# Performance work log

Hardware: AMD Instinct MI355X
Metric: run time of the kernel (lower is better)

The kernel has to match this reference:

```python
import jax, jax.numpy as jnp
import numpy as np
from jax import lax

EPS = 1e-5
TEM = 10.0  # self.tem at init; tem_proportion buffer is 0 so it stays 10.0


def _conv1d(x, w, padding, dilation=1, groups=1):
    # x: [B, C, S], w: [O, I//groups, K]
    return lax.conv_general_dilated(
        x, w, window_strides=(1,), padding=[(padding, padding)],
        rhs_dilation=(dilation,), dimension_numbers=('NCH', 'OIH', 'NCH'),
        feature_group_count=groups)


def _bn(y, gamma, beta):
    # training-mode BatchNorm1d: stats over (batch, length) per channel
    m = y.mean(axis=(0, 2), keepdims=True)
    v = y.var(axis=(0, 2), keepdims=True)
    return (y - m) * lax.rsqrt(v + EPS) * gamma[None, :, None] + beta[None, :, None]


def _nor_conv(x, w, g, b, k):
    return _bn(_conv1d(jax.nn.relu(x), w, padding=k // 2), g, b)


def _dil_conv(x, wd, wp, g, b, k):
    C = x.shape[1]
    y = _conv1d(jax.nn.relu(x), wd, padding=k - 1, dilation=2, groups=C)
    y = _conv1d(y, wp, padding=0)
    return _bn(y, g, b)


def _avg_pool3(x):
    s = lax.reduce_window(x, 0.0, lax.add, (1, 1, 3), (1, 1, 1),
                          [(0, 0), (0, 0), (1, 1)])
    return s / 3.0  # count_include_pad=True


def _max_pool3(x):
    return lax.reduce_window(x, -jnp.inf, lax.max, (1, 1, 3), (1, 1, 1),
                             [(0, 0), (0, 0), (1, 1)])


def _forward(x, u, arch_parameters,
             w_nor3, g_nor3, b_nor3, w_nor5, g_nor5, b_nor5,
             w_nor7, g_nor7, b_nor7,
             wd_dil3, wp_dil3, g_dil3, b_dil3,
             wd_dil5, wp_dil5, g_dil5, b_dil5,
             wd_dil7, wp_dil7, g_dil7, b_dil7):
    # ---- Gumbel straight-through gate (get_gumbel_prob) ----
    uc = jnp.clip(u, 1e-9, 1.0 - 1e-9)
    gumbels = -jnp.log(-jnp.log(uc))  # -log(Exp(1) sample)
    logits = (jax.nn.log_softmax(arch_parameters, axis=1) + gumbels) / TEM
    probs = jax.nn.softmax(logits, axis=1)          # [1, 10]
    index = jnp.argmax(probs, axis=-1)              # [1]
    one_h = jax.nn.one_hot(index, probs.shape[-1], dtype=probs.dtype)
    hardwts = one_h - lax.stop_gradient(probs) + probs  # straight-through

    # ---- forward_gdas: single edge (max_nodes=2) ----
    xc = jnp.transpose(x, (0, 2, 1))  # [B, H, S]: hidden=channels, seq=length
    branches = [
        lambda t: jnp.zeros_like(t),                         # none
        _avg_pool3,                                          # avg_pool_3
        _max_pool3,                                          # max_pool_3
        lambda t: _nor_conv(t, w_nor3, g_nor3, b_nor3, 3),   # nor_conv_3
        lambda t: _nor_conv(t, w_nor5, g_nor5, b_nor5, 5),   # nor_conv_5
        lambda t: _nor_conv(t, w_nor7, g_nor7, b_nor7, 7),   # nor_conv_7
        lambda t: _dil_conv(t, wd_dil3, wp_dil3, g_dil3, b_dil3, 3),
        lambda t: _dil_conv(t, wd_dil5, wp_dil5, g_dil5, b_dil5, 5),
        lambda t: _dil_conv(t, wd_dil7, wp_dil7, g_dil7, b_dil7, 7),
        lambda t: t,                                         # skip_connect
    ]
    idx = index[0]
    w = hardwts[0]                                  # [10]
    sel = lax.switch(idx, branches, xc)             # only argmax op is run
    w_sel = jnp.take(w, idx)
    # GDAS: w[argmax]*op(x) + sum of remaining scalar weights (broadcast add)
    out = w_sel * sel + (jnp.sum(w) - w_sel)
    out = jnp.transpose(out, (0, 2, 1))             # back to [B, S, H]
    return out + x                                  # residual


def setup_inputs() -> dict:
    key = jax.random.key(0)
    ks = jax.random.split(key, 16)
    B, S, H = 8, 512, 768
    d = {
        'x': jax.random.normal(ks[0], (B, S, H), jnp.float32),
        'u': jax.random.uniform(ks[1], (1, 10), jnp.float32),
        'arch_parameters': 0.001 * jax.random.normal(ks[2], (1, 10), jnp.float32),
    }
    i = 3
    for k in (3, 5, 7):
        d[f'w_nor{k}'] = 0.02 * jax.random.normal(ks[i], (H, H, k), jnp.float32); i += 1
        d[f'g_nor{k}'] = jnp.ones((H,), jnp.float32)
        d[f'b_nor{k}'] = jnp.zeros((H,), jnp.float32)
    for k in (3, 5, 7):
        d[f'wd_dil{k}'] = 0.1 * jax.random.normal(ks[i], (H, 1, k), jnp.float32); i += 1
        d[f'wp_dil{k}'] = 0.02 * jax.random.normal(ks[i], (H, H, 1), jnp.float32); i += 1
        d[f'g_dil{k}'] = jnp.ones((H,), jnp.float32)
        d[f'b_dil{k}'] = jnp.zeros((H,), jnp.float32)
    return d


def reference(x, u, arch_parameters,
              w_nor3, g_nor3, b_nor3, w_nor5, g_nor5, b_nor5,
              w_nor7, g_nor7, b_nor7,
              wd_dil3, wp_dil3, g_dil3, b_dil3,
              wd_dil5, wp_dil5, g_dil5, b_dil5,
              wd_dil7, wp_dil7, g_dil7, b_dil7):
    return _forward(x, u, arch_parameters,
                    w_nor3, g_nor3, b_nor3, w_nor5, g_nor5, b_nor5,
                    w_nor7, g_nor7, b_nor7,
                    wd_dil3, wp_dil3, g_dil3, b_dil3,
                    wd_dil5, wp_dil5, g_dil5, b_dil5,
                    wd_dil7, wp_dil7, g_dil7, b_dil7)
```

## Files before the change

### kernel.cpp

```cpp
#include <hip/hip_runtime.h>
#include <math.h>

#define BB 8
#define SS 512
#define HH 768
#define NTOT (BB*SS*HH)
#define EPSBN 1e-5f

typedef __attribute__((ext_vector_type(8))) short short8v;
typedef __attribute__((ext_vector_type(4))) float float4v;

struct Params {
  const float *x, *u, *ap;
  const float *w_nor3, *g_nor3, *b_nor3;
  const float *w_nor5, *g_nor5, *b_nor5;
  const float *w_nor7, *g_nor7, *b_nor7;
  const float *wd3, *wp3, *gd3, *bd3;
  const float *wd5, *wp5, *gd5, *bd5;
  const float *wd7, *wp7, *gd7, *bd7;
  float *out;
  float *hdr;
  float *y;
  float *z;
  float *psum;
  float *psq;
  float *mbuf;
  float *ibuf;
};

__device__ __forceinline__ short f2bf(float f) {
  union { float f; unsigned u; } v; v.f = f;
  unsigned r = v.u + 0x7FFF + ((v.u >> 16) & 1);
  return (short)(r >> 16);
}

__global__ void gate_kernel(Params p) {
  if (threadIdx.x != 0 || blockIdx.x != 0) return;
  float ap[10], lg[10], pr[10];
  float mx = -INFINITY;
  for (int i = 0; i < 10; i++) { ap[i] = p.ap[i]; mx = fmaxf(mx, ap[i]); }
  float se = 0.f;
  for (int i = 0; i < 10; i++) se += expf(ap[i] - mx);
  float lse = mx + logf(se);
  float lmax = -INFINITY;
  for (int i = 0; i < 10; i++) {
    float uc = fminf(fmaxf(p.u[i], 1e-9f), 1.f - 1e-9f);
    float gb = -logf(-logf(uc));
    lg[i] = ((ap[i] - lse) + gb) * 0.1f;
    lmax = fmaxf(lmax, lg[i]);
  }
  float ps = 0.f;
  for (int i = 0; i < 10; i++) { pr[i] = expf(lg[i] - lmax); ps += pr[i]; }
  int idx = 0; float best = -INFINITY;
  for (int i = 0; i < 10; i++) {
    pr[i] /= ps;
    if (pr[i] > best) { best = pr[i]; idx = i; }
  }
  float w_sel = (1.0f - pr[idx]) + pr[idx];
  p.hdr[0] = w_sel;
  p.hdr[1] = 0.0f;
  ((int*)p.hdr)[2] = idx;
}

__global__ __launch_bounds__(256) void dw_kernel(Params p) {
  int idx = ((const int*)p.hdr)[2];
  if (idx < 6 || idx > 8) return;
  int k = 3 + 2 * (idx - 6);
  const float* wd = (idx == 6) ? p.wd3 : (idx == 7) ? p.wd5 : p.wd7;
  int tid = blockIdx.x * 256 + threadIdx.x;
  if (tid >= NTOT) return;
  int c = tid % HH;
  int bs = tid / HH;
  int s = bs % SS;
  int b = bs / SS;
  float acc = 0.f;
  for (int dk = 0; dk < k; dk++) {
    int ss = s + 2 * dk - (k - 1);
    if (ss >= 0 && ss < SS) {
      float v = p.x[((size_t)(b * SS + ss)) * HH + c];
      acc += fmaxf(v, 0.f) * wd[c * k + dk];
    }
  }
  p.z[tid] = acc;
}

#define BM 128
#define BN 64
#define BK 32
#define LROW 40
__global__ __launch_bounds__(256) void conv_gemm_kernel(Params p) {
  int idx = ((const int*)p.hdr)[2];
  if (idx < 3 || idx > 8) return;
  bool nor = (idx <= 5);
  int k = nor ? (3 + 2 * (idx - 3)) : (3 + 2 * (idx - 6));
  const float* W = nor ? ((idx == 3) ? p.w_nor3 : (idx == 4) ? p.w_nor5 : p.w_nor7)
                       : ((idx == 6) ? p.wp3 : (idx == 7) ? p.wp5 : p.wp7);
  const float* A = nor ? p.x : p.z;
  int taps = nor ? k : 1;
  int halo = nor ? (k >> 1) : 0;

  __shared__ __attribute__((aligned(16))) short As[BM * LROW];
  __shared__ __attribute__((aligned(16))) short Bs[BN * LROW];

  int mt = blockIdx.x;
  int b = mt >> 2;
  int s0 = (mt & 3) * BM;
  int o0 = blockIdx.y * BN;

  int t = threadIdx.x;
  int lane = t & 63;
  int wid = t >> 6;
  int wm0 = (wid >> 1) * 64;
  int wn0 = (wid & 1) * 32;
  int l16 = lane & 15;
  int quad = lane >> 4;

  int sa_m = t >> 1;
  int sa_h = t & 1;
  int sb_n = t >> 2;
  int sb_seg = t & 3;

  float4v acc[4][2];
#pragma unroll
  for (int mi = 0; mi < 4; mi++)
#pragma unroll
    for (int ni = 0; ni < 2; ni++) acc[mi][ni] = (float4v){0.f, 0.f, 0.f, 0.f};

  for (int dk = 0; dk < taps; dk++) {
    int shift = dk - halo;
    for (int k0 = 0; k0 < HH; k0 += BK) {
      {
        int srow = s0 + sa_m + shift;
        float4 f[4];
        if (srow >= 0 && srow < SS) {
          const float* ap = A + ((size_t)(b * SS + srow)) * HH + k0 + sa_h * 16;
#pragma unroll
          for (int j = 0; j < 4; j++) f[j] = ((const float4*)ap)[j];
        } else {
#pragma unroll
          for (int j = 0; j < 4; j++) f[j] = (float4){0.f, 0.f, 0.f, 0.f};
        }
        short h16[16];
#pragma unroll
        for (int j = 0; j < 4; j++) {
          float vx = f[j].x, vy = f[j].y, vz = f[j].z, vw = f[j].w;
          if (nor) { vx = fmaxf(vx, 0.f); vy = fmaxf(vy, 0.f); vz = fmaxf(vz, 0.f); vw = fmaxf(vw, 0.f); }
          h16[4 * j + 0] = f2bf(vx); h16[4 * j + 1] = f2bf(vy);
          h16[4 * j + 2] = f2bf(vz); h16[4 * j + 3] = f2bf(vw);
        }
        short* dst = &As[sa_m * LROW + sa_h * 16];
        *(short8v*)dst = *(short8v*)&h16[0];
        *(short8v*)(dst + 8) = *(short8v*)&h16[8];
      }
      {
        short h8[8];
        int o = o0 + sb_n;
        if (!nor) {
          const float* bp = W + (size_t)o * HH + k0 + sb_seg * 8;
          float4 f0 = ((const float4*)bp)[0];
          float4 f1 = ((const float4*)bp)[1];
          h8[0] = f2bf(f0.x); h8[1] = f2bf(f0.y); h8[2] = f2bf(f0.z); h8[3] = f2bf(f0.w);
          h8[4] = f2bf(f1.x); h8[5] = f2bf(f1.y); h8[6] = f2bf(f1.z); h8[7] = f2bf(f1.w);
        } else {
#pragma unroll
          for (int j = 0; j < 8; j++) {
            int i = k0 + sb_seg * 8 + j;
            h8[j] = f2bf(W[((size_t)o * HH + i) * k + dk]);
          }
        }
        *(short8v*)&Bs[sb_n * LROW + sb_seg * 8] = *(short8v*)&h8[0];
      }
      __syncthreads();

      short8v af[4], bf[2];
#pragma unroll
      for (int mi = 0; mi < 4; mi++)
        af[mi] = *(const short8v*)&As[(wm0 + mi * 16 + l16) * LROW + quad * 8];
#pragma unroll
      for (int ni = 0; ni < 2; ni++)
        bf[ni] = *(const short8v*)&Bs[(wn0 + ni * 16 + l16) * LROW + quad * 8];
#pragma unroll
      for (int mi = 0; mi < 4; mi++)
#pragma unroll
        for (int ni = 0; ni < 2; ni++)
          acc[mi][ni] = __builtin_amdgcn_mfma_f32_16x16x32_bf16(af[mi], bf[ni], acc[mi][ni], 0, 0, 0);
      __syncthreads();
    }
  }

#pragma unroll
  for (int mi = 0; mi < 4; mi++) {
#pragma unroll
    for (int ni = 0; ni < 2; ni++) {
      int col = o0 + wn0 + ni * 16 + l16;
#pragma unroll
      for (int r = 0; r < 4; r++) {
        int row = s0 + wm0 + mi * 16 + quad * 4 + r;
        p.y[((size_t)(b * SS + row)) * HH + col] = acc[mi][ni][r];
      }
    }
  }
}

__global__ __launch_bounds__(256) void bn_stats1(Params p) {
  int idx = ((const int*)p.hdr)[2];
  if (idx < 3 || idx > 8) return;
  int t = threadIdx.x;
  int c = blockIdx.y * 64 + (t & 63);
  int rsub = t >> 6;
  float s = 0.f, q = 0.f;
  int rbase = blockIdx.x * 256 + rsub;
  for (int j = 0; j < 64; j++) {
    float v = p.y[(size_t)(rbase + 4 * j) * HH + c];
    s += v; q += v * v;
  }
  __shared__ float red[2][4][64];
  red[0][rsub][t & 63] = s;
  red[1][rsub][t & 63] = q;
  __syncthreads();
  if (t < 64) {
    float ts = red[0][0][t] + red[0][1][t] + red[0][2][t] + red[0][3][t];
    float tq = red[1][0][t] + red[1][1][t] + red[1][2][t] + red[1][3][t];
    p.psum[blockIdx.x * HH + blockIdx.y * 64 + t] = ts;
    p.psq[blockIdx.x * HH + blockIdx.y * 64 + t] = tq;
  }
}

__global__ __launch_bounds__(256) void bn_stats2(Params p) {
  int idx = ((const int*)p.hdr)[2];
  if (idx < 3 || idx > 8) return;
  int c = blockIdx.x * 256 + threadIdx.x;
  if (c >= HH) return;
  float s = 0.f, q = 0.f;
  for (int j = 0; j < 16; j++) { s += p.psum[j * HH + c]; q += p.psq[j * HH + c]; }
  float mean = s * (1.f / 4096.f);
  float var = q * (1.f / 4096.f) - mean * mean;
  p.mbuf[c] = mean;
  p.ibuf[c] = rsqrtf(var + EPSBN);
}

__global__ __launch_bounds__(256) void epilogue_kernel(Params p) {
  int idx = ((const int*)p.hdr)[2];
  float w_sel = p.hdr[0], w_rest = p.hdr[1];
  int tid = blockIdx.x * 256 + threadIdx.x;
  if (tid >= NTOT) return;
  float xv = p.x[tid];
  float sel;
  if (idx >= 3 && idx <= 8) {
    const float* g = (idx == 3) ? p.g_nor3 : (idx == 4) ? p.g_nor5 : (idx == 5) ? p.g_nor7
                   : (idx == 6) ? p.gd3 : (idx == 7) ? p.gd5 : p.gd7;
    const float* be = (idx == 3) ? p.b_nor3 : (idx == 4) ? p.b_nor5 : (idx == 5) ? p.b_nor7
                    : (idx == 6) ? p.bd3 : (idx == 7) ? p.bd5 : p.bd7;
    int h = tid % HH;
    float yv = p.y[tid];
    sel = (yv - p.mbuf[h]) * p.ibuf[h] * g[h] + be[h];
  } else if (idx == 0) {
    sel = 0.f;
  } else if (idx == 9) {
    sel = xv;
  } else {
    int bs = tid / HH;
    int s = bs % SS;
    if (idx == 1) {
      float xm = (s > 0) ? p.x[tid - HH] : 0.f;
      float xp = (s < SS - 1) ? p.x[tid + HH] : 0.f;
      sel = (xm + xv + xp) * (1.f / 3.f);
    } else {
      float xm = (s > 0) ? p.x[tid - HH] : -INFINITY;
      float xp = (s < SS - 1) ? p.x[tid + HH] : -INFINITY;
      sel = fmaxf(fmaxf(xm, xv), xp);
    }
  }
  p.out[tid] = w_sel * sel + w_rest + xv;
}

extern "C" void kernel_launch(void* const* d_in, const int* in_sizes, int n_in,
                              void* d_out, int out_size, void* d_ws, size_t ws_size,
                              hipStream_t stream) {
  Params p;
  p.x = (const float*)d_in[0];
  p.u = (const float*)d_in[1];
  p.ap = (const float*)d_in[2];
  p.w_nor3 = (const float*)d_in[3];  p.g_nor3 = (const float*)d_in[4];  p.b_nor3 = (const float*)d_in[5];
  p.w_nor5 = (const float*)d_in[6];  p.g_nor5 = (const float*)d_in[7];  p.b_nor5 = (const float*)d_in[8];
  p.w_nor7 = (const float*)d_in[9];  p.g_nor7 = (const float*)d_in[10]; p.b_nor7 = (const float*)d_in[11];
  p.wd3 = (const float*)d_in[12]; p.wp3 = (const float*)d_in[13]; p.gd3 = (const float*)d_in[14]; p.bd3 = (const float*)d_in[15];
  p.wd5 = (const float*)d_in[16]; p.wp5 = (const float*)d_in[17]; p.gd5 = (const float*)d_in[18]; p.bd5 = (const float*)d_in[19];
  p.wd7 = (const float*)d_in[20]; p.wp7 = (const float*)d_in[21]; p.gd7 = (const float*)d_in[22]; p.bd7 = (const float*)d_in[23];
  p.out = (float*)d_out;

  char* ws = (char*)d_ws;
  size_t off = 0;
  p.hdr = (float*)(ws + off); off += 256;
  p.y   = (float*)(ws + off); off += (size_t)NTOT * 4;
  p.z   = (float*)(ws + off); off += (size_t)NTOT * 4;
  p.psum = (float*)(ws + off); off += 16 * HH * 4;
  p.psq  = (float*)(ws + off); off += 16 * HH * 4;
  p.mbuf = (float*)(ws + off); off += HH * 4;
  p.ibuf = (float*)(ws + off); off += HH * 4;

  int nblk = (NTOT + 255) / 256;

  hipLaunchKernelGGL(gate_kernel, dim3(1), dim3(64), 0, stream, p);
  hipLaunchKernelGGL(dw_kernel, dim3(nblk), dim3(256), 0, stream, p);
  hipLaunchKernelGGL(conv_gemm_kernel, dim3(32, HH / BN), dim3(256), 0, stream, p);
  hipLaunchKernelGGL(bn_stats1, dim3(16, HH / 64), dim3(256), 0, stream, p);
  hipLaunchKernelGGL(bn_stats2, dim3((HH + 255) / 256), dim3(256), 0, stream, p);
  hipLaunchKernelGGL(epilogue_kernel, dim3(nblk), dim3(256), 0, stream, p);
}
```

Baseline: 144.7 us.

## Merge all stages into one cooperative persistent kernel with grid syncs

Replaces the six separate launches (gate, depthwise, GEMM, two BN-stat passes, epilogue) with a single cooperative kernel of 512 blocks that recomputes the Gumbel gate in every block and separates phases with grid-wide syncs. For the parameter-free branches it skips the GEMM and BN work entirely and writes output in one vectorized pass. The GEMM tile shrinks from 128x64 to 64x64 and is scheduled persistently over 768 tiles, and the elementwise passes use float4. Grid syncs and the smaller tiles with less reuse could offset the savings from fewer launches.

New measurement: 176.1 us. +21.7%, slower.

```diff
diff --git a/kernel.cpp b/kernel.cpp
--- a/kernel.cpp
+++ b/kernel.cpp
@@ -1,11 +1,18 @@
 #include <hip/hip_runtime.h>
+#include <hip/hip_cooperative_groups.h>
 #include <math.h>
+
+namespace cg = cooperative_groups;
 
 #define BB 8
 #define SS 512
 #define HH 768
+#define H4 (HH/4)
 #define NTOT (BB*SS*HH)
+#define N4 (NTOT/4)
 #define EPSBN 1e-5f
+#define GRID 512
+#define TPB 256
 
 typedef __attribute__((ext_vector_type(8))) short short8v;
 typedef __attribute__((ext_vector_type(4))) float float4v;
@@ -19,7 +26,6 @@
   const float *wd5, *wp5, *gd5, *bd5;
   const float *wd7, *wp7, *gd7, *bd7;
   float *out;
-  float *hdr;
   float *y;
   float *z;
   float *psum;
@@ -34,244 +40,253 @@
   return (short)(r >> 16);
 }
 
-__global__ void gate_kernel(Params p) {
-  if (threadIdx.x != 0 || blockIdx.x != 0) return;
-  float ap[10], lg[10], pr[10];
+__global__ __launch_bounds__(TPB, 2) void nas_coop(Params p) {
+  cg::grid_group gg = cg::this_grid();
+  int t = threadIdx.x;
+  int bid = blockIdx.x;
+
+  float apv[10], lg[10], pr[10];
   float mx = -INFINITY;
-  for (int i = 0; i < 10; i++) { ap[i] = p.ap[i]; mx = fmaxf(mx, ap[i]); }
+#pragma unroll
+  for (int i = 0; i < 10; i++) { apv[i] = p.ap[i]; mx = fmaxf(mx, apv[i]); }
   float se = 0.f;
-  for (int i = 0; i < 10; i++) se += expf(ap[i] - mx);
+#pragma unroll
+  for (int i = 0; i < 10; i++) se += expf(apv[i] - mx);
   float lse = mx + logf(se);
   float lmax = -INFINITY;
+#pragma unroll
   for (int i = 0; i < 10; i++) {
     float uc = fminf(fmaxf(p.u[i], 1e-9f), 1.f - 1e-9f);
     float gb = -logf(-logf(uc));
-    lg[i] = ((ap[i] - lse) + gb) * 0.1f;
+    lg[i] = ((apv[i] - lse) + gb) * 0.1f;
     lmax = fmaxf(lmax, lg[i]);
   }
   float ps = 0.f;
+#pragma unroll
   for (int i = 0; i < 10; i++) { pr[i] = expf(lg[i] - lmax); ps += pr[i]; }
   int idx = 0; float best = -INFINITY;
+#pragma unroll
   for (int i = 0; i < 10; i++) {
     pr[i] /= ps;
     if (pr[i] > best) { best = pr[i]; idx = i; }
   }
   float w_sel = (1.0f - pr[idx]) + pr[idx];
-  p.hdr[0] = w_sel;
-  p.hdr[1] = 0.0f;
-  ((int*)p.hdr)[2] = idx;
-}
-
-__global__ __launch_bounds__(256) void dw_kernel(Params p) {
-  int idx = ((const int*)p.hdr)[2];
-  if (idx < 6 || idx > 8) return;
-  int k = 3 + 2 * (idx - 6);
-  const float* wd = (idx == 6) ? p.wd3 : (idx == 7) ? p.wd5 : p.wd7;
-  int tid = blockIdx.x * 256 + threadIdx.x;
-  if (tid >= NTOT) return;
-  int c = tid % HH;
-  int bs = tid / HH;
-  int s = bs % SS;
-  int b = bs / SS;
-  float acc = 0.f;
-  for (int dk = 0; dk < k; dk++) {
-    int ss = s + 2 * dk - (k - 1);
-    if (ss >= 0 && ss < SS) {
-      float v = p.x[((size_t)(b * SS + ss)) * HH + c];
-      acc += fmaxf(v, 0.f) * wd[c * k + dk];
-    }
-  }
-  p.z[tid] = acc;
-}
-
-#define BM 128
-#define BN 64
-#define BK 32
-#define LROW 40
-__global__ __launch_bounds__(256) void conv_gemm_kernel(Params p) {
-  int idx = ((const int*)p.hdr)[2];
-  if (idx < 3 || idx > 8) return;
+
+  const float4* x4 = (const float4*)p.x;
+  float4* o4 = (float4*)p.out;
+
+  if (idx < 3 || idx > 8) {
+    for (int i = bid * TPB + t; i < N4; i += GRID * TPB) {
+      float4 xv = x4[i];
+      float4 sel;
+      if (idx == 0) {
+        sel = make_float4(0.f, 0.f, 0.f, 0.f);
+      } else if (idx == 9) {
+        sel = xv;
+      } else {
+        int row = i / H4;
+        int s = row % SS;
+        if (idx == 1) {
+          float4 xm = (s > 0) ? x4[i - H4] : make_float4(0.f, 0.f, 0.f, 0.f);
+          float4 xp = (s < SS - 1) ? x4[i + H4] : make_float4(0.f, 0.f, 0.f, 0.f);
+          sel.x = (xm.x + xv.x + xp.x) * (1.f / 3.f);
+          sel.y = (xm.y + xv.y + xp.y) * (1.f / 3.f);
+          sel.z = (xm.z + xv.z + xp.z) * (1.f / 3.f);
+          sel.w = (xm.w + xv.w + xp.w) * (1.f / 3.f);
+        } else {
+          float4 xm = (s > 0) ? x4[i - H4] : make_float4(-INFINITY, -INFINITY, -INFINITY, -INFINITY);
+          float4 xp = (s < SS - 1) ? x4[i + H4] : make_float4(-INFINITY, -INFINITY, -INFINITY, -INFINITY);
+          sel.x = fmaxf(fmaxf(xm.x, xv.x), xp.x);
+          sel.y = fmaxf(fmaxf(xm.y, xv.y), xp.y);
+          sel.z = fmaxf(fmaxf(xm.z, xv.z), xp.z);
+          sel.w = fmaxf(fmaxf(xm.w, xv.w), xp.w);
+        }
+      }
+      float4 ov;
+      ov.x = w_sel * sel.x + xv.x;
+      ov.y = w_sel * sel.y + xv.y;
+      ov.z = w_sel * sel.z + xv.z;
+      ov.w = w_sel * sel.w + xv.w;
+      o4[i] = ov;
+    }
+    return;
+  }
+
   bool nor = (idx <= 5);
   int k = nor ? (3 + 2 * (idx - 3)) : (3 + 2 * (idx - 6));
+
+  __shared__ __attribute__((aligned(16))) short lds[2 * 64 * 40];
+  short* As = lds;
+  short* Bs = lds + 64 * 40;
+
+  if (!nor) {
+    const float* wd = (idx == 6) ? p.wd3 : (idx == 7) ? p.wd5 : p.wd7;
+    float4* z4 = (float4*)p.z;
+    for (int i = bid * TPB + t; i < N4; i += GRID * TPB) {
+      int row = i / H4;
+      int c0 = (i - row * H4) * 4;
+      int s = row % SS;
+      int b = row / SS;
+      float4 acc = make_float4(0.f, 0.f, 0.f, 0.f);
+      for (int dk = 0; dk < k; dk++) {
+        int ss = s + 2 * dk - (k - 1);
+        if (ss >= 0 && ss < SS) {
+          float4 xv = x4[(b * SS + ss) * H4 + (c0 >> 2)];
+          acc.x += fmaxf(xv.x, 0.f) * wd[(c0 + 0) * k + dk];
+          acc.y += fmaxf(xv.y, 0.f) * wd[(c0 + 1) * k + dk];
+          acc.z += fmaxf(xv.z, 0.f) * wd[(c0 + 2) * k + dk];
+          acc.w += fmaxf(xv.w, 0.f) * wd[(c0 + 3) * k + dk];
+        }
+      }
+      z4[i] = acc;
+    }
+    gg.sync();
+  }
+
   const float* W = nor ? ((idx == 3) ? p.w_nor3 : (idx == 4) ? p.w_nor5 : p.w_nor7)
                        : ((idx == 6) ? p.wp3 : (idx == 7) ? p.wp5 : p.wp7);
   const float* A = nor ? p.x : p.z;
   int taps = nor ? k : 1;
   int halo = nor ? (k >> 1) : 0;
 
-  __shared__ __attribute__((aligned(16))) short As[BM * LROW];
-  __shared__ __attribute__((aligned(16))) short Bs[BN * LROW];
-
-  int mt = blockIdx.x;
-  int b = mt >> 2;
-  int s0 = (mt & 3) * BM;
-  int o0 = blockIdx.y * BN;
-
-  int t = threadIdx.x;
-  int lane = t & 63;
-  int wid = t >> 6;
-  int wm0 = (wid >> 1) * 64;
-  int wn0 = (wid & 1) * 32;
-  int l16 = lane & 15;
-  int quad = lane >> 4;
-
-  int sa_m = t >> 1;
-  int sa_h = t & 1;
-  int sb_n = t >> 2;
-  int sb_seg = t & 3;
-
-  float4v acc[4][2];
-#pragma unroll
-  for (int mi = 0; mi < 4; mi++)
-#pragma unroll
-    for (int ni = 0; ni < 2; ni++) acc[mi][ni] = (float4v){0.f, 0.f, 0.f, 0.f};
-
-  for (int dk = 0; dk < taps; dk++) {
-    int shift = dk - halo;
-    for (int k0 = 0; k0 < HH; k0 += BK) {
-      {
-        int srow = s0 + sa_m + shift;
-        float4 f[4];
-        if (srow >= 0 && srow < SS) {
-          const float* ap = A + ((size_t)(b * SS + srow)) * HH + k0 + sa_h * 16;
-#pragma unroll
-          for (int j = 0; j < 4; j++) f[j] = ((const float4*)ap)[j];
-        } else {
-#pragma unroll
-          for (int j = 0; j < 4; j++) f[j] = (float4){0.f, 0.f, 0.f, 0.f};
-        }
-        short h16[16];
-#pragma unroll
-        for (int j = 0; j < 4; j++) {
-          float vx = f[j].x, vy = f[j].y, vz = f[j].z, vw = f[j].w;
-          if (nor) { vx = fmaxf(vx, 0.f); vy = fmaxf(vy, 0.f); vz = fmaxf(vz, 0.f); vw = fmaxf(vw, 0.f); }
-          h16[4 * j + 0] = f2bf(vx); h16[4 * j + 1] = f2bf(vy);
-          h16[4 * j + 2] = f2bf(vz); h16[4 * j + 3] = f2bf(vw);
-        }
-        short* dst = &As[sa_m * LROW + sa_h * 16];
-        *(short8v*)dst = *(short8v*)&h16[0];
-        *(short8v*)(dst + 8) = *(short8v*)&h16[8];
-      }
-      {
-        short h8[8];
-        int o = o0 + sb_n;
-        if (!nor) {
-          const float* bp = W + (size_t)o * HH + k0 + sb_seg * 8;
-          float4 f0 = ((const float4*)bp)[0];
-          float4 f1 = ((const float4*)bp)[1];
+  int lane = t & 63, wid = t >> 6;
+  int wm0 = (wid >> 1) * 32, wn0 = (wid & 1) * 32;
+  int l16 = lane & 15, quad = lane >> 4;
+  int s_row = t >> 2, s_seg = t & 3;
+
+  for (int tile = bid; tile < 64 * 12; tile += GRID) {
+    int mt = tile & 63, nt = tile >> 6;
+    int b = mt >> 3, s0 = (mt & 7) * 64, o0 = nt * 64;
+    float4v acc[2][2];
+#pragma unroll
+    for (int mi = 0; mi < 2; mi++)
+#pragma unroll
+      for (int ni = 0; ni < 2; ni++) acc[mi][ni] = (float4v){0.f, 0.f, 0.f, 0.f};
+
+    for (int dk = 0; dk < taps; dk++) {
+      int shift = dk - halo;
+      for (int k0 = 0; k0 < HH; k0 += 32) {
+        {
+          int srow = s0 + s_row + shift;
+          float4 f0, f1;
+          if (srow >= 0 && srow < SS) {
+            const float* apt = A + ((size_t)(b * SS + srow)) * HH + k0 + s_seg * 8;
+            f0 = ((const float4*)apt)[0];
+            f1 = ((const float4*)apt)[1];
+          } else {
+            f0 = make_float4(0.f, 0.f, 0.f, 0.f);
+            f1 = f0;
+          }
+          if (nor) {
+            f0.x = fmaxf(f0.x, 0.f); f0.y = fmaxf(f0.y, 0.f); f0.z = fmaxf(f0.z, 0.f); f0.w = fmaxf(f0.w, 0.f);
+            f1.x = fmaxf(f1.x, 0.f); f1.y = fmaxf(f1.y, 0.f); f1.z = fmaxf(f1.z, 0.f); f1.w = fmaxf(f1.w, 0.f);
+          }
+          short h8[8];
           h8[0] = f2bf(f0.x); h8[1] = f2bf(f0.y); h8[2] = f2bf(f0.z); h8[3] = f2bf(f0.w);
           h8[4] = f2bf(f1.x); h8[5] = f2bf(f1.y); h8[6] = f2bf(f1.z); h8[7] = f2bf(f1.w);
-        } else {
-#pragma unroll
-          for (int j = 0; j < 8; j++) {
-            int i = k0 + sb_seg * 8 + j;
-            h8[j] = f2bf(W[((size_t)o * HH + i) * k + dk]);
+          *(short8v*)&As[s_row * 40 + s_seg * 8] = *(short8v*)&h8[0];
+        }
+        {
+          int o = o0 + s_row;
+          short hb[8];
+          if (!nor) {
+            const float* bp = W + (size_t)o * HH + k0 + s_seg * 8;
+            float4 g0 = ((const float4*)bp)[0];
+            float4 g1 = ((const float4*)bp)[1];
+            hb[0] = f2bf(g0.x); hb[1] = f2bf(g0.y); hb[2] = f2bf(g0.z); hb[3] = f2bf(g0.w);
+            hb[4] = f2bf(g1.x); hb[5] = f2bf(g1.y); hb[6] = f2bf(g1.z); hb[7] = f2bf(g1.w);
+          } else {
+#pragma unroll
+            for (int j = 0; j < 8; j++)
+              hb[j] = f2bf(W[((size_t)o * HH + k0 + s_seg * 8 + j) * k + dk]);
           }
-        }
-        *(short8v*)&Bs[sb_n * LROW + sb_seg * 8] = *(short8v*)&h8[0];
+          *(short8v*)&Bs[s_row * 40 + s_seg * 8] = *(short8v*)&hb[0];
+        }
+        __syncthreads();
+        short8v af[2], bf[2];
+#pragma unroll
+        for (int mi = 0; mi < 2; mi++)
+          af[mi] = *(const short8v*)&As[(wm0 + mi * 16 + l16) * 40 + quad * 8];
+#pragma unroll
+        for (int ni = 0; ni < 2; ni++)
+          bf[ni] = *(const short8v*)&Bs[(wn0 + ni * 16 + l16) * 40 + quad * 8];
+#pragma unroll
+        for (int mi = 0; mi < 2; mi++)
+#pragma unroll
+          for (int ni = 0; ni < 2; ni++)
+            acc[mi][ni] = __builtin_amdgcn_mfma_f32_16x16x32_bf16(af[mi], bf[ni], acc[mi][ni], 0, 0, 0);
+        __syncthreads();
       }
-      __syncthreads();
-
-      short8v af[4], bf[2];
-#pragma unroll
-      for (int mi = 0; mi < 4; mi++)
-        af[mi] = *(const short8v*)&As[(wm0 + mi * 16 + l16) * LROW + quad * 8];
-#pragma unroll
-      for (int ni = 0; ni < 2; ni++)
-        bf[ni] = *(const short8v*)&Bs[(wn0 + ni * 16 + l16) * LROW + quad * 8];
-#pragma unroll
-      for (int mi = 0; mi < 4; mi++)
-#pragma unroll
-        for (int ni = 0; ni < 2; ni++)
-          acc[mi][ni] = __builtin_amdgcn_mfma_f32_16x16x32_bf16(af[mi], bf[ni], acc[mi][ni], 0, 0, 0);
-      __syncthreads();
-    }
-  }
-
-#pragma unroll
-  for (int mi = 0; mi < 4; mi++) {
-#pragma unroll
-    for (int ni = 0; ni < 2; ni++) {
-      int col = o0 + wn0 + ni * 16 + l16;
-#pragma unroll
-      for (int r = 0; r < 4; r++) {
-        int row = s0 + wm0 + mi * 16 + quad * 4 + r;
-        p.y[((size_t)(b * SS + row)) * HH + col] = acc[mi][ni][r];
+    }
+#pragma unroll
+    for (int mi = 0; mi < 2; mi++)
+#pragma unroll
+      for (int ni = 0; ni < 2; ni++) {
+        int col = o0 + wn0 + ni * 16 + l16;
+#pragma unroll
+        for (int r = 0; r < 4; r++) {
+          int row = s0 + wm0 + mi * 16 + quad * 4 + r;
+          p.y[((size_t)(b * SS + row)) * HH + col] = acc[mi][ni][r];
+        }
       }
-    }
-  }
-}
-
-__global__ __launch_bounds__(256) void bn_stats1(Params p) {
-  int idx = ((const int*)p.hdr)[2];
-  if (idx < 3 || idx > 8) return;
-  int t = threadIdx.x;
-  int c = blockIdx.y * 64 + (t & 63);
-  int rsub = t >> 6;
-  float s = 0.f, q = 0.f;
-  int rbase = blockIdx.x * 256 + rsub;
-  for (int j = 0; j < 64; j++) {
-    float v = p.y[(size_t)(rbase + 4 * j) * HH + c];
-    s += v; q += v * v;
-  }
-  __shared__ float red[2][4][64];
-  red[0][rsub][t & 63] = s;
-  red[1][rsub][t & 63] = q;
-  __syncthreads();
-  if (t < 64) {
-    float ts = red[0][0][t] + red[0][1][t] + red[0][2][t] + red[0][3][t];
-    float tq = red[1][0][t] + red[1][1][t] + red[1][2][t] + red[1][3][t];
-    p.psum[blockIdx.x * HH + blockIdx.y * 64 + t] = ts;
-    p.psq[blockIdx.x * HH + blockIdx.y * 64 + t] = tq;
-  }
-}
-
-__global__ __launch_bounds__(256) void bn_stats2(Params p) {
-  int idx = ((const int*)p.hdr)[2];
-  if (idx < 3 || idx > 8) return;
-  int c = blockIdx.x * 256 + threadIdx.x;
-  if (c >= HH) return;
-  float s = 0.f, q = 0.f;
-  for (int j = 0; j < 16; j++) { s += p.psum[j * HH + c]; q += p.psq[j * HH + c]; }
-  float mean = s * (1.f / 4096.f);
-  float var = q * (1.f / 4096.f) - mean * mean;
-  p.mbuf[c] = mean;
-  p.ibuf[c] = rsqrtf(var + EPSBN);
-}
-
-__global__ __launch_bounds__(256) void epilogue_kernel(Params p) {
-  int idx = ((const int*)p.hdr)[2];
-  float w_sel = p.hdr[0], w_rest = p.hdr[1];
-  int tid = blockIdx.x * 256 + threadIdx.x;
-  if (tid >= NTOT) return;
-  float xv = p.x[tid];
-  float sel;
-  if (idx >= 3 && idx <= 8) {
+  }
+  gg.sync();
+
+  if (bid < 192) {
+    int rchunk = bid & 15, cgp = bid >> 4;
+    int c = cgp * 64 + (t & 63);
+    int rsub = t >> 6;
+    float s_ = 0.f, q = 0.f;
+    int rbase = rchunk * 256 + rsub;
+    for (int j = 0; j < 64; j++) {
+      float v = p.y[(size_t)(rbase + 4 * j) * HH + c];
+      s_ += v; q += v * v;
+    }
+    float* red = (float*)lds;
+    red[(0 * 4 + rsub) * 64 + (t & 63)] = s_;
+    red[(1 * 4 + rsub) * 64 + (t & 63)] = q;
+    __syncthreads();
+    if (t < 64) {
+      float ts = red[t] + red[64 + t] + red[128 + t] + red[192 + t];
+      float tq = red[256 + t] + red[320 + t] + red[384 + t] + red[448 + t];
+      p.psum[rchunk * HH + cgp * 64 + t] = ts;
+      p.psq[rchunk * HH + cgp * 64 + t] = tq;
+    }
+  }
+  gg.sync();
+
+  if (bid < 3) {
+    int c = bid * TPB + t;
+    float s_ = 0.f, q = 0.f;
+    for (int j = 0; j < 16; j++) { s_ += p.psum[j * HH + c]; q += p.psq[j * HH + c]; }
+    float mean = s_ * (1.f / 4096.f);
+    float var = q * (1.f / 4096.f) - mean * mean;
+    p.mbuf[c] = mean;
+    p.ibuf[c] = rsqrtf(var + EPSBN);
+  }
+  gg.sync();
+
+  {
     const float* g = (idx == 3) ? p.g_nor3 : (idx == 4) ? p.g_nor5 : (idx == 5) ? p.g_nor7
                    : (idx == 6) ? p.gd3 : (idx == 7) ? p.gd5 : p.gd7;
     const float* be = (idx == 3) ? p.b_nor3 : (idx == 4) ? p.b_nor5 : (idx == 5) ? p.b_nor7
                     : (idx == 6) ? p.bd3 : (idx == 7) ? p.bd5 : p.bd7;
-    int h = tid % HH;
-    float yv = p.y[tid];
-    sel = (yv - p.mbuf[h]) * p.ibuf[h] * g[h] + be[h];
-  } else if (idx == 0) {
-    sel = 0.f;
-  } else if (idx == 9) {
-    sel = xv;
-  } else {
-    int bs = tid / HH;
-    int s = bs % SS;
-    if (idx == 1) {
-      float xm = (s > 0) ? p.x[tid - HH] : 0.f;
-      float xp = (s < SS - 1) ? p.x[tid + HH] : 0.f;
-      sel = (xm + xv + xp) * (1.f / 3.f);
-    } else {
-      float xm = (s > 0) ? p.x[tid - HH] : -INFINITY;
-      float xp = (s < SS - 1) ? p.x[tid + HH] : -INFINITY;
-      sel = fmaxf(fmaxf(xm, xv), xp);
-    }
-  }
-  p.out[tid] = w_sel * sel + w_rest + xv;
+    const float4* y4 = (const float4*)p.y;
+    for (int i = bid * TPB + t; i < N4; i += GRID * TPB) {
+      int c0 = (i % H4) * 4;
+      float4 xv = x4[i], yv = y4[i];
+      float4 sel, ov;
+      sel.x = (yv.x - p.mbuf[c0 + 0]) * p.ibuf[c0 + 0] * g[c0 + 0] + be[c0 + 0];
+      sel.y = (yv.y - p.mbuf[c0 + 1]) * p.ibuf[c0 + 1] * g[c0 + 1] + be[c0 + 1];
+      sel.z = (yv.z - p.mbuf[c0 + 2]) * p.ibuf[c0 + 2] * g[c0 + 2] + be[c0 + 2];
+      sel.w = (yv.w - p.mbuf[c0 + 3]) * p.ibuf[c0 + 3] * g[c0 + 3] + be[c0 + 3];
+      ov.x = w_sel * sel.x + xv.x;
+      ov.y = w_sel * sel.y + xv.y;
+      ov.z = w_sel * sel.z + xv.z;
+      ov.w = w_sel * sel.w + xv.w;
+      o4[i] = ov;
+    }
+  }
 }
 
 extern "C" void kernel_launch(void* const* d_in, const int* in_sizes, int n_in,
@@ -291,7 +306,6 @@
 
   char* ws = (char*)d_ws;
   size_t off = 0;
-  p.hdr = (float*)(ws + off); off += 256;
   p.y   = (float*)(ws + off); off += (size_t)NTOT * 4;
   p.z   = (float*)(ws + off); off += (size_t)NTOT * 4;
   p.psum = (float*)(ws + off); off += 16 * HH * 4;
@@ -299,12 +313,8 @@
   p.mbuf = (float*)(ws + off); off += HH * 4;
   p.ibuf = (float*)(ws + off); off += HH * 4;
 
-  int nblk = (NTOT + 255) / 256;
-
-  hipLaunchKernelGGL(gate_kernel, dim3(1), dim3(64), 0, stream, p);
-  hipLaunchKernelGGL(dw_kernel, dim3(nblk), dim3(256), 0, stream, p);
-  hipLaunchKernelGGL(conv_gemm_kernel, dim3(32, HH / BN), dim3(256), 0, stream, p);
-  hipLaunchKernelGGL(bn_stats1, dim3(16, HH / 64), dim3(256), 0, stream, p);
-  hipLaunchKernelGGL(bn_stats2, dim3((HH + 255) / 256), dim3(256), 0, stream, p);
-  hipLaunchKernelGGL(epilogue_kernel, dim3(nblk), dim3(256), 0, stream, p);
+  Params* pp = &p;
+  void* args[] = { (void*)pp };
+  hipLaunchCooperativeKernel((const void*)nas_coop, dim3(GRID), dim3(TPB),
+                             args, 0, stream);
 }
```
